# Kernel tuning notes

Hardware: AMD Instinct MI355X
Metric: run time of the kernel (lower is better)

The kernel has to match this reference:

```python
import jax, jax.numpy as jnp
import numpy as np

H = 2048          # hidden_size
M = 512           # moe_intermediate_size
E = 8             # n_routed_experts
TOP_K = 2         # num_experts_per_tok
N_SHARED = 2      # n_shared_experts -> shared intermediate = M * N_SHARED
MS = M * N_SHARED
B, S = 2, 1024


def setup_inputs() -> dict:
    key = jax.random.key(0)
    ks = jax.random.split(key, 9)
    sc = 0.02
    return {
        "hidden_states": jax.random.normal(ks[0], (B, S, H), dtype=jnp.float32),
        "gate_w": jax.random.normal(ks[1], (E, H), dtype=jnp.float32) * sc,
        "Wg": jax.random.normal(ks[2], (E, H, M), dtype=jnp.float32) * sc,   # gate_proj per expert
        "Wu": jax.random.normal(ks[3], (E, H, M), dtype=jnp.float32) * sc,   # up_proj per expert
        "Wd": jax.random.normal(ks[4], (E, M, H), dtype=jnp.float32) * sc,   # down_proj per expert
        "sWg": jax.random.normal(ks[5], (H, MS), dtype=jnp.float32) * sc,    # shared gate_proj
        "sWu": jax.random.normal(ks[6], (H, MS), dtype=jnp.float32) * sc,    # shared up_proj
        "sWd": jax.random.normal(ks[7], (MS, H), dtype=jnp.float32) * sc,    # shared down_proj
    }


def reference(hidden_states, gate_w, Wg, Wu, Wd, sWg, sWu, sWd):
    b, s, h = hidden_states.shape
    x = hidden_states.reshape(-1, h)                     # [N, H]
    n = x.shape[0]

    # --- MoEGate: top-k routing with softmax over the selected logits ---
    logits = x @ gate_w.T                                # [N, E]
    topk_vals, topk_idx = jax.lax.top_k(logits, TOP_K)   # [N, K]
    w = jax.nn.softmax(topk_vals, axis=-1)               # softmax scoring over top-k
    # per-token combine weight for every expert (zero where not routed)
    comb = jnp.zeros((n, E), x.dtype).at[jnp.arange(n)[:, None], topk_idx].add(w)

    # --- Routed experts (SwiGLU MLP per expert); combine is the sparse
    #     weight matrix `comb`, mathematically identical to torch dispatch ---
    g = jnp.einsum('nh,ehm->enm', x, Wg)                 # [E, N, M]
    u = jnp.einsum('nh,ehm->enm', x, Wu)
    eo = jnp.einsum('enm,emh->enh', jax.nn.silu(g) * u, Wd)  # [E, N, H]
    y = jnp.einsum('ne,enh->nh', comb, eo)               # weighted combine

    # --- Shared experts (dense SwiGLU MLP on all tokens) ---
    y = y + (jax.nn.silu(x @ sWg) * (x @ sWu)) @ sWd
    return y.reshape(b, s, h)
```

## Files before the change

### kernel.cpp

```cpp
#include <hip/hip_runtime.h>

#define H 2048
#define MDIM 512
#define NE 8
#define MS 1024
#define NTOK 2048
#define ACT_R_ROWS 5120

typedef unsigned short u16;
typedef __attribute__((ext_vector_type(4))) short s16x4;
typedef __attribute__((ext_vector_type(8))) short s16x8;
typedef __attribute__((ext_vector_type(4))) float f32x4;

__device__ inline u16 f2bf(float f) {
  unsigned u = __builtin_bit_cast(unsigned, f);
  u = (u + 0x7fffu + ((u >> 16) & 1u)) >> 16;
  return (u16)u;
}
__device__ inline float bf2f(u16 v) {
  return __builtin_bit_cast(float, (unsigned)v << 16);
}

__device__ inline f32x4 mfma16(s16x8 a, s16x8 b, f32x4 c) {
  return __builtin_amdgcn_mfma_f32_16x16x32_bf16(a, b, c, 0, 0, 0);
}

__device__ inline void gload16(const void* g, void* l) {
  __builtin_amdgcn_global_load_lds(
      (const __attribute__((address_space(1))) unsigned int*)g,
      (__attribute__((address_space(3))) unsigned int*)l, 16, 0, 0);
}


__device__ inline void tile_t64(const float* __restrict__ src, u16* __restrict__ dst,
                                int R, int C, int bx, int by, u16 (*tt)[66]) {
  int c0 = bx * 64, r0 = by * 64;
  int t = threadIdx.x;
  int cq = (t & 15) * 4, rr = t >> 4;
  #pragma unroll
  for (int i = 0; i < 4; i++) {
    int row = rr + i * 16;
    f32x4 v = *(const f32x4*)&src[(long)(r0 + row) * C + c0 + cq];
    tt[cq + 0][row] = f2bf(v[0]);
    tt[cq + 1][row] = f2bf(v[1]);
    tt[cq + 2][row] = f2bf(v[2]);
    tt[cq + 3][row] = f2bf(v[3]);
  }
  __syncthreads();
  int c = t >> 2, ch = t & 3;
  #pragma unroll
  for (int h = 0; h < 2; h++) {
    int chunk = ch + h * 4;
    const u16* p = &tt[c][chunk * 8];
    s16x8 o;
    #pragma unroll
    for (int w0 = 0; w0 < 8; w0++) o[w0] = (short)p[w0];
    *(s16x8*)&dst[(long)(c0 + c) * R + r0 + chunk * 8] = o;
  }
}

__global__ __launch_bounds__(256) void k_front(
    const float* __restrict__ x, const float* __restrict__ gw,
    u16* __restrict__ xbf, int* __restrict__ te, float* __restrict__ tw,
    const float* __restrict__ Wg, const float* __restrict__ Wu,
    const float* __restrict__ Wd, const float* __restrict__ sWg,
    const float* __restrict__ sWu, const float* __restrict__ sWd,
    u16* __restrict__ WgT, u16* __restrict__ WuT, u16* __restrict__ WdT,
    u16* __restrict__ sWgT, u16* __restrict__ sWuT, u16* __restrict__ sWdT) {
  __shared__ u16 tt[64][66];
  int blk = blockIdx.x;
  if (blk < NTOK / 4) {
    int n = blk * 4 + (threadIdx.x >> 6);
    int lane = threadIdx.x & 63;
    double acc[NE];
    #pragma unroll
    for (int e = 0; e < NE; e++) acc[e] = 0.0;
    const f32x4* xr = (const f32x4*)(x + (size_t)n * H);
    s16x4* xo = (s16x4*)(xbf + (size_t)n * H);
    #pragma unroll
    for (int it = 0; it < H / 256; it++) {
      int j4 = it * 64 + lane;
      f32x4 v = xr[j4];
      s16x4 o;
      o[0] = (short)f2bf(v[0]); o[1] = (short)f2bf(v[1]);
      o[2] = (short)f2bf(v[2]); o[3] = (short)f2bf(v[3]);
      xo[j4] = o;
      #pragma unroll
      for (int e = 0; e < NE; e++) {
        f32x4 g = *(const f32x4*)&gw[e * H + j4 * 4];
        acc[e] += (double)v[0] * g[0] + (double)v[1] * g[1] +
                  (double)v[2] * g[2] + (double)v[3] * g[3];
      }
    }
    #pragma unroll
    for (int off = 32; off; off >>= 1) {
      #pragma unroll
      for (int e = 0; e < NE; e++) acc[e] += __shfl_xor(acc[e], off);
    }
    if (lane == 0) {
      int b0 = 0; double v0 = acc[0];
      #pragma unroll
      for (int e = 1; e < NE; e++) { if (acc[e] > v0) { v0 = acc[e]; b0 = e; } }
      int b1 = -1; double v1 = -1e300;
      #pragma unroll
      for (int e = 0; e < NE; e++) { if (e != b0 && acc[e] > v1) { v1 = acc[e]; b1 = e; } }
      double ex = exp(v1 - v0);
      te[n * 2] = b0; te[n * 2 + 1] = b1;
      tw[n * 2] = (float)(1.0 / (1.0 + ex));
      tw[n * 2 + 1] = (float)(ex / (1.0 + ex));
    }
    return;
  }
  int b = blk - NTOK / 4;
  const float* src; u16* dst; int R, C, lb;
  if (b < 2048) {
    lb = b; R = H; C = MDIM;
    int z = lb >> 8; lb &= 255;
    src = Wg + (size_t)z * H * MDIM; dst = WgT + (size_t)z * MDIM * H;
  } else if (b < 4096) {
    lb = b - 2048; R = H; C = MDIM;
    int z = lb >> 8; lb &= 255;
    src = Wu + (size_t)z * H * MDIM; dst = WuT + (size_t)z * MDIM * H;
  } else if (b < 6144) {
    lb = b - 4096; R = MDIM; C = H;
    int z = lb >> 8; lb &= 255;
    src = Wd + (size_t)z * MDIM * H; dst = WdT + (size_t)z * H * MDIM;
  } else if (b < 6656) {
    lb = b - 6144; R = H; C = MS; src = sWg; dst = sWgT;
  } else if (b < 7168) {
    lb = b - 6656; R = H; C = MS; src = sWu; dst = sWuT;
  } else {
    lb = b - 7168; R = MS; C = H; src = sWd; dst = sWdT;
  }
  int nbx = C >> 6;
  tile_t64(src, dst, R, C, lb % nbx, lb / nbx, tt);
}

__global__ __launch_bounds__(256) void k_build(
    const int* __restrict__ te, const float* __restrict__ tw,
    int* __restrict__ counts, int* __restrict__ offs,
    int* __restrict__ perm, float* __restrict__ wgt, int* __restrict__ slotmap) {
  __shared__ int cnt[256][NE];
  __shared__ int pb[NE];
  int t = threadIdx.x;
  int ebuf[16];
  int lc[NE];
  #pragma unroll
  for (int e = 0; e < NE; e++) lc[e] = 0;
  #pragma unroll
  for (int i = 0; i < 16; i++) {
    int ei = te[t * 16 + i];
    ebuf[i] = ei;
    #pragma unroll
    for (int e = 0; e < NE; e++) lc[e] += (ei == e) ? 1 : 0;
  }
  #pragma unroll
  for (int e = 0; e < NE; e++) cnt[t][e] = lc[e];
  __syncthreads();
  if (t < NE) {
    int run = 0;
    for (int i = 0; i < 256; i++) { int v = cnt[i][t]; cnt[i][t] = run; run += v; }
    counts[t] = run;
  }
  __syncthreads();
  if (t == 0) {
    int off = 0;
    #pragma unroll
    for (int e = 0; e < NE; e++) {
      pb[e] = off; offs[e] = off;
      off += ((counts[e] + 127) >> 7) << 7;
    }
    offs[NE] = off;
  }
  for (int i = t; i < ACT_R_ROWS; i += 256) { perm[i] = 0; wgt[i] = 0.f; }
  __syncthreads();
  int run2[NE];
  #pragma unroll
  for (int e = 0; e < NE; e++) run2[e] = cnt[t][e];
  #pragma unroll
  for (int i = 0; i < 16; i++) {
    int ei = ebuf[i];
    int idx = 0;
    #pragma unroll
    for (int e = 0; e < NE; e++) {
      if (ei == e) idx = pb[e] + run2[e];
      run2[e] += (ei == e) ? 1 : 0;
    }
    perm[idx] = (t * 16 + i) >> 1;
    wgt[idx] = tw[t * 16 + i];
    slotmap[t * 16 + i] = idx;
  }
}

__global__ __launch_bounds__(256, 2) void k_gu(
    const u16* __restrict__ xbf, const u16* __restrict__ WgT, const u16* __restrict__ WuT,
    const u16* __restrict__ sWgT, const u16* __restrict__ sWuT,
    u16* __restrict__ act_s, u16* __restrict__ act_r,
    const int* __restrict__ perm, const int* __restrict__ counts,
    const int* __restrict__ offs) {
  int lin = blockIdx.x;
  int xcd = lin & 7, jj = lin >> 3;
  int g = xcd + 8 * (jj % 10);
  int bx = jj / 10;
  const u16 *Bg, *Bu;
  u16* act;
  int Nout, cnt, rowBase, by;
  bool gather;
  if (g < 16) {
    gather = false; by = g;
    cnt = NTOK; rowBase = bx * 128;
    Bg = sWgT + (size_t)by * 64 * H;
    Bu = sWuT + (size_t)by * 64 * H;
    act = act_s; Nout = MS;
  } else {
    gather = true;
    int e = (g - 16) >> 3; by = (g - 16) & 7;
    cnt = counts[e];
    if (bx * 128 >= cnt) return;
    rowBase = offs[e] + bx * 128;
    Bg = WgT + ((size_t)e * MDIM + (size_t)by * 64) * H;
    Bu = WuT + ((size_t)e * MDIM + (size_t)by * 64) * H;
    act = act_r; Nout = MDIM;
  }

  __shared__ char lds[2][32768];

  int tid = threadIdx.x;
  int wave = tid >> 6, lane = tid & 63;
  int wr = wave >> 1, wc = wave & 1;
  int la = lane & 15, ks = lane >> 4;

  int rIn = tid >> 3;
  int csrc = ((tid & 7) << 4) ^ ((rIn & 7) << 4);
  const char* srcA[4];
  const char* srcBg[2];
  const char* srcBu[2];
  #pragma unroll
  for (int j = 0; j < 4; j++) {
    int row = j * 32 + rIn;
    int tok = gather ? perm[rowBase + row] : (rowBase + row);
    srcA[j] = (const char*)xbf + (size_t)tok * H * 2 + csrc;
  }
  #pragma unroll
  for (int j = 0; j < 2; j++) {
    int row = j * 32 + rIn;
    srcBg[j] = (const char*)Bg + (size_t)row * H * 2 + csrc;
    srcBu[j] = (const char*)Bu + (size_t)row * H * 2 + csrc;
  }

  int offA[4][2], offB[2][2];
  #pragma unroll
  for (int m = 0; m < 4; m++) {
    int arow = wr * 64 + m * 16 + la;
    #pragma unroll
    for (int kk = 0; kk < 2; kk++) {
      int c = kk * 64 + ks * 16;
      offA[m][kk] = arow * 128 + (c ^ ((arow & 7) << 4));
    }
  }
  #pragma unroll
  for (int n = 0; n < 2; n++) {
    int brow = wc * 32 + n * 16 + la;
    #pragma unroll
    for (int kk = 0; kk < 2; kk++) {
      int c = kk * 64 + ks * 16;
      offB[n][kk] = brow * 128 + (c ^ ((brow & 7) << 4));
    }
  }

  f32x4 zero4 = {0.f, 0.f, 0.f, 0.f};
  f32x4 gacc[4][2], uacc[4][2];
  #pragma unroll
  for (int m = 0; m < 4; m++)
    #pragma unroll
    for (int n = 0; n < 2; n++) { gacc[m][n] = zero4; uacc[m][n] = zero4; }

  auto STAGE = [&](int p, int k0) {
    char* b = lds[p];
    #pragma unroll
    for (int j = 0; j < 4; j++)
      gload16(srcA[j] + k0, b + j * 4096 + wave * 1024);
    #pragma unroll
    for (int j = 0; j < 2; j++) {
      gload16(srcBg[j] + k0, b + 16384 + j * 4096 + wave * 1024);
      gload16(srcBu[j] + k0, b + 24576 + j * 4096 + wave * 1024);
    }
  };

  const int NT = H / 64;
  STAGE(0, 0);
  STAGE(1, 128);
  asm volatile("s_waitcnt vmcnt(8)" ::: "memory");
  __builtin_amdgcn_sched_barrier(0);
  __builtin_amdgcn_s_barrier();

  for (int t = 0; t < NT; ++t) {
    int p = t & 1;
    const char* A = lds[p];
    const char* G = lds[p] + 16384;
    const char* U = lds[p] + 24576;
    s16x8 af[2][4], gf[2][2], uf[2][2];
    #pragma unroll
    for (int kk = 0; kk < 2; kk++) {
      #pragma unroll
      for (int m = 0; m < 4; m++) af[kk][m] = *(const s16x8*)(A + offA[m][kk]);
      #pragma unroll
      for (int n = 0; n < 2; n++) {
        gf[kk][n] = *(const s16x8*)(G + offB[n][kk]);
        uf[kk][n] = *(const s16x8*)(U + offB[n][kk]);
      }
    }
    asm volatile("s_waitcnt lgkmcnt(0)" ::: "memory");
    __builtin_amdgcn_sched_barrier(0);
    __builtin_amdgcn_s_barrier();
    if (t + 2 < NT) STAGE(p, (t + 2) * 128);
    __builtin_amdgcn_sched_barrier(0);
    __builtin_amdgcn_s_setprio(1);
    #pragma unroll
    for (int kk = 0; kk < 2; kk++) {
      #pragma unroll
      for (int m = 0; m < 4; m++) {
        #pragma unroll
        for (int n = 0; n < 2; n++) {
          gacc[m][n] = mfma16(af[kk][m], gf[kk][n], gacc[m][n]);
          uacc[m][n] = mfma16(af[kk][m], uf[kk][n], uacc[m][n]);
        }
      }
    }
    __builtin_amdgcn_s_setprio(0);
    if (t + 2 < NT) { asm volatile("s_waitcnt vmcnt(8)" ::: "memory"); }
    else            { asm volatile("s_waitcnt vmcnt(0)" ::: "memory"); }
    __builtin_amdgcn_sched_barrier(0);
    __builtin_amdgcn_s_barrier();
  }

  #pragma unroll
  for (int m = 0; m < 4; m++) {
    #pragma unroll
    for (int n = 0; n < 2; n++) {
      #pragma unroll
      for (int r = 0; r < 4; r++) {
        int lr = wr * 64 + m * 16 + ks * 4 + r;
        int col = by * 64 + wc * 32 + n * 16 + la;
        float gg = gacc[m][n][r], uu = uacc[m][n][r];
        float a = gg / (1.0f + __expf(-gg)) * uu;
        if (gather && (bx * 128 + lr) >= cnt) a = 0.0f;
        act[(size_t)(rowBase + lr) * Nout + col] = f2bf(a);
      }
    }
  }
}

__global__ __launch_bounds__(256, 3) void k_down2(
    const u16* __restrict__ act_s, const u16* __restrict__ act_r,
    const u16* __restrict__ sWdT, const u16* __restrict__ WdT,
    float* __restrict__ y, u16* __restrict__ rdown,
    const float* __restrict__ wgt,
    const int* __restrict__ counts, const int* __restrict__ offs) {
  int lin = blockIdx.x;
  int xcd = lin & 7, jj = lin >> 3;
  int g = xcd + 8 * (jj % 36);
  int bx = jj / 36;
  const u16 *A, *B;
  int KD, NT, cnt, rowBase, by;
  bool routed;
  if (g < 32) {
    routed = false; by = g;
    KD = MS; NT = MS / 64;
    cnt = NTOK; rowBase = bx * 128;
    A = act_s + (size_t)rowBase * MS;
    B = sWdT + (size_t)by * 64 * MS;
  } else {
    routed = true;
    int e = (g - 32) >> 5; by = (g - 32) & 31;
    KD = MDIM; NT = MDIM / 64;
    cnt = counts[e];
    if (bx * 128 >= cnt) return;
    rowBase = offs[e] + bx * 128;
    A = act_r + (size_t)rowBase * MDIM;
    B = WdT + ((size_t)e * H + (size_t)by * 64) * MDIM;
  }

  __shared__ char lds[2][24576];

  int tid = threadIdx.x;
  int wave = tid >> 6, lane = tid & 63;
  int wr = wave >> 1, wc = wave & 1;
  int la = lane & 15, ks = lane >> 4;

  int rIn = tid >> 3;
  int csrc = ((tid & 7) << 4) ^ ((rIn & 7) << 4);
  const char* srcA[4];
  const char* srcB[2];
  #pragma unroll
  for (int j = 0; j < 4; j++) {
    int row = j * 32 + rIn;
    srcA[j] = (const char*)A + (size_t)row * KD * 2 + csrc;
  }
  #pragma unroll
  for (int j = 0; j < 2; j++) {
    int row = j * 32 + rIn;
    srcB[j] = (const char*)B + (size_t)row * KD * 2 + csrc;
  }

  int offA[4][2], offB[2][2];
  #pragma unroll
  for (int m = 0; m < 4; m++) {
    int arow = wr * 64 + m * 16 + la;
    #pragma unroll
    for (int kk = 0; kk < 2; kk++) {
      int c = kk * 64 + ks * 16;
      offA[m][kk] = arow * 128 + (c ^ ((arow & 7) << 4));
    }
  }
  #pragma unroll
  for (int n = 0; n < 2; n++) {
    int brow = wc * 32 + n * 16 + la;
    #pragma unroll
    for (int kk = 0; kk < 2; kk++) {
      int c = kk * 64 + ks * 16;
      offB[n][kk] = brow * 128 + (c ^ ((brow & 7) << 4));
    }
  }

  f32x4 zero4 = {0.f, 0.f, 0.f, 0.f};
  f32x4 acc[4][2];
  #pragma unroll
  for (int m = 0; m < 4; m++)
    #pragma unroll
    for (int n = 0; n < 2; n++) acc[m][n] = zero4;

  auto STAGE = [&](int p, int k0) {
    char* b = lds[p];
    #pragma unroll
    for (int j = 0; j < 4; j++)
      gload16(srcA[j] + k0, b + j * 4096 + wave * 1024);
    #pragma unroll
    for (int j = 0; j < 2; j++)
      gload16(srcB[j] + k0, b + 16384 + j * 4096 + wave * 1024);
  };

  STAGE(0, 0);
  STAGE(1, 128);
  asm volatile("s_waitcnt vmcnt(6)" ::: "memory");
  __builtin_amdgcn_sched_barrier(0);
  __builtin_amdgcn_s_barrier();

  for (int t = 0; t < NT; ++t) {
    int p = t & 1;
    const char* Ab = lds[p];
    const char* Bb = lds[p] + 16384;
    s16x8 af[2][4], bf[2][2];
    #pragma unroll
    for (int kk = 0; kk < 2; kk++) {
      #pragma unroll
      for (int m = 0; m < 4; m++) af[kk][m] = *(const s16x8*)(Ab + offA[m][kk]);
      #pragma unroll
      for (int n = 0; n < 2; n++) bf[kk][n] = *(const s16x8*)(Bb + offB[n][kk]);
    }
    asm volatile("s_waitcnt lgkmcnt(0)" ::: "memory");
    __builtin_amdgcn_sched_barrier(0);
    __builtin_amdgcn_s_barrier();
    if (t + 2 < NT) STAGE(p, (t + 2) * 128);
    __builtin_amdgcn_sched_barrier(0);
    __builtin_amdgcn_s_setprio(1);
    #pragma unroll
    for (int kk = 0; kk < 2; kk++) {
      #pragma unroll
      for (int m = 0; m < 4; m++)
        #pragma unroll
        for (int n = 0; n < 2; n++) acc[m][n] = mfma16(af[kk][m], bf[kk][n], acc[m][n]);
    }
    __builtin_amdgcn_s_setprio(0);
    if (t + 2 < NT) { asm volatile("s_waitcnt vmcnt(6)" ::: "memory"); }
    else            { asm volatile("s_waitcnt vmcnt(0)" ::: "memory"); }
    __builtin_amdgcn_sched_barrier(0);
    __builtin_amdgcn_s_barrier();
  }

  #pragma unroll
  for (int m = 0; m < 4; m++) {
    #pragma unroll
    for (int n = 0; n < 2; n++) {
      #pragma unroll
      for (int r = 0; r < 4; r++) {
        int lr = wr * 64 + m * 16 + ks * 4 + r;
        int col = by * 64 + wc * 32 + n * 16 + la;
        float v = acc[m][n][r];
        if (routed) {
          if (bx * 128 + lr < cnt) {
            int si = rowBase + lr;
            rdown[(size_t)si * H + col] = f2bf(wgt[si] * v);
          }
        } else {
          y[(size_t)(rowBase + lr) * H + col] = v;
        }
      }
    }
  }
}

__global__ __launch_bounds__(256) void k_combine(float* __restrict__ y,
                                                 const u16* __restrict__ rdown,
                                                 const int* __restrict__ slotmap) {
  int n = blockIdx.x;
  int s0 = slotmap[n * 2], s1 = slotmap[n * 2 + 1];
  const s16x8* r0 = (const s16x8*)(rdown + (size_t)s0 * H);
  const s16x8* r1 = (const s16x8*)(rdown + (size_t)s1 * H);
  f32x4* yp = (f32x4*)(y + (size_t)n * H);
  int t = threadIdx.x;
  s16x8 a = r0[t], b = r1[t];
  f32x4 y0 = yp[2 * t], y1 = yp[2 * t + 1];
  #pragma unroll
  for (int j = 0; j < 4; j++) {
    y0[j] += bf2f((u16)a[j]) + bf2f((u16)b[j]);
    y1[j] += bf2f((u16)a[4 + j]) + bf2f((u16)b[4 + j]);
  }
  yp[2 * t] = y0;
  yp[2 * t + 1] = y1;
}


extern "C" void kernel_launch(void* const* d_in, const int* in_sizes, int n_in,
                              void* d_out, int out_size, void* d_ws, size_t ws_size,
                              hipStream_t stream) {
  const float* x   = (const float*)d_in[0];
  const float* gw  = (const float*)d_in[1];
  const float* Wg  = (const float*)d_in[2];
  const float* Wu  = (const float*)d_in[3];
  const float* Wd  = (const float*)d_in[4];
  const float* sWg = (const float*)d_in[5];
  const float* sWu = (const float*)d_in[6];
  const float* sWd = (const float*)d_in[7];
  float* y = (float*)d_out;

  char* w = (char*)d_ws;
  auto alloc = [&](size_t bytes) {
    char* p = w;
    w += (bytes + 255) & ~(size_t)255;
    return p;
  };
  u16* xbf   = (u16*)alloc((size_t)NTOK * H * 2);
  u16* WgT   = (u16*)alloc((size_t)NE * MDIM * H * 2);
  u16* WuT   = (u16*)alloc((size_t)NE * MDIM * H * 2);
  u16* WdT   = (u16*)alloc((size_t)NE * H * MDIM * 2);
  u16* sWgT  = (u16*)alloc((size_t)MS * H * 2);
  u16* sWuT  = (u16*)alloc((size_t)MS * H * 2);
  u16* sWdT  = (u16*)alloc((size_t)H * MS * 2);
  u16* act_s = (u16*)alloc((size_t)NTOK * MS * 2);
  u16* act_r = (u16*)alloc((size_t)ACT_R_ROWS * MDIM * 2);
  u16* rdown = (u16*)alloc((size_t)ACT_R_ROWS * H * 2);
  int*   te      = (int*)alloc((size_t)NTOK * 2 * 4);
  float* tw      = (float*)alloc((size_t)NTOK * 2 * 4);
  int*   counts  = (int*)alloc(64);
  int*   offs    = (int*)alloc(64);
  int*   perm    = (int*)alloc((size_t)ACT_R_ROWS * 4);
  float* wgt     = (float*)alloc((size_t)ACT_R_ROWS * 4);
  int*   slotmap = (int*)alloc((size_t)NTOK * 2 * 4);

  k_front<<<NTOK / 4 + 7680, 256, 0, stream>>>(
      x, gw, xbf, te, tw, Wg, Wu, Wd, sWg, sWu, sWd,
      WgT, WuT, WdT, sWgT, sWuT, sWdT);

  k_build<<<1, 256, 0, stream>>>(te, tw, counts, offs, perm, wgt, slotmap);

  k_gu<<<80 * 16, 256, 0, stream>>>(
      xbf, WgT, WuT, sWgT, sWuT, act_s, act_r, perm, counts, offs);

  k_down2<<<288 * 16, 256, 0, stream>>>(
      act_s, act_r, sWdT, WdT, y, rdown, wgt, counts, offs);

  k_combine<<<NTOK, 256, 0, stream>>>(y, rdown, slotmap);
}
```

Before: 149.0 us.

## Switch GEMM kernels to 4-stage LDS ring with K=32 tiles

Both the gate/up and down GEMM kernels change from a 2-buffer, K=64-per-step pipeline to a 4-buffer ring with K=32 per step, prefetching 3 tiles ahead. This removes one barrier per iteration, since the next stage is issued into a buffer nobody is reading, and the LDS swizzle is redone for 64-byte rows. The aim is deeper latency hiding with the same LDS footprint. The cost is twice as many loop iterations with fewer MFMAs each, and the wait counts must match the deeper prefetch exactly.

Measured after the change: 159.1 us. +6.8%, slower.

```diff
diff --git a/kernel.cpp b/kernel.cpp
--- a/kernel.cpp
+++ b/kernel.cpp
@@ -223,49 +223,37 @@
     act = act_r; Nout = MDIM;
   }
 
-  __shared__ char lds[2][32768];
+  __shared__ char lds[4][16384];
 
   int tid = threadIdx.x;
   int wave = tid >> 6, lane = tid & 63;
   int wr = wave >> 1, wc = wave & 1;
   int la = lane & 15, ks = lane >> 4;
 
-  int rIn = tid >> 3;
-  int csrc = ((tid & 7) << 4) ^ ((rIn & 7) << 4);
-  const char* srcA[4];
-  const char* srcBg[2];
-  const char* srcBu[2];
-  #pragma unroll
-  for (int j = 0; j < 4; j++) {
-    int row = j * 32 + rIn;
+  const char* srcA[2];
+  #pragma unroll
+  for (int j = 0; j < 2; j++) {
+    int idx = tid + j * 256;
+    int row = idx >> 2;
+    int gc = (idx & 3) ^ ((row >> 1) & 3);
     int tok = gather ? perm[rowBase + row] : (rowBase + row);
-    srcA[j] = (const char*)xbf + (size_t)tok * H * 2 + csrc;
-  }
-  #pragma unroll
-  for (int j = 0; j < 2; j++) {
-    int row = j * 32 + rIn;
-    srcBg[j] = (const char*)Bg + (size_t)row * H * 2 + csrc;
-    srcBu[j] = (const char*)Bu + (size_t)row * H * 2 + csrc;
-  }
-
-  int offA[4][2], offB[2][2];
+    srcA[j] = (const char*)xbf + (size_t)tok * H * 2 + gc * 16;
+  }
+  int rowB = tid >> 2;
+  int gcB = (tid & 3) ^ ((rowB >> 1) & 3);
+  const char* srcBg = (const char*)Bg + (size_t)rowB * H * 2 + gcB * 16;
+  const char* srcBu = (const char*)Bu + (size_t)rowB * H * 2 + gcB * 16;
+
+  int offA[4], offB[2];
   #pragma unroll
   for (int m = 0; m < 4; m++) {
     int arow = wr * 64 + m * 16 + la;
-    #pragma unroll
-    for (int kk = 0; kk < 2; kk++) {
-      int c = kk * 64 + ks * 16;
-      offA[m][kk] = arow * 128 + (c ^ ((arow & 7) << 4));
-    }
+    offA[m] = (arow * 4 + (ks ^ ((arow >> 1) & 3))) * 16;
   }
   #pragma unroll
   for (int n = 0; n < 2; n++) {
     int brow = wc * 32 + n * 16 + la;
-    #pragma unroll
-    for (int kk = 0; kk < 2; kk++) {
-      int c = kk * 64 + ks * 16;
-      offB[n][kk] = brow * 128 + (c ^ ((brow & 7) << 4));
-    }
+    offB[n] = (brow * 4 + (ks ^ ((brow >> 1) & 3))) * 16;
   }
 
   f32x4 zero4 = {0.f, 0.f, 0.f, 0.f};
@@ -277,58 +265,44 @@
 
   auto STAGE = [&](int p, int k0) {
     char* b = lds[p];
-    #pragma unroll
-    for (int j = 0; j < 4; j++)
-      gload16(srcA[j] + k0, b + j * 4096 + wave * 1024);
-    #pragma unroll
-    for (int j = 0; j < 2; j++) {
-      gload16(srcBg[j] + k0, b + 16384 + j * 4096 + wave * 1024);
-      gload16(srcBu[j] + k0, b + 24576 + j * 4096 + wave * 1024);
-    }
+    gload16(srcA[0] + k0, b + wave * 1024);
+    gload16(srcA[1] + k0, b + 4096 + wave * 1024);
+    gload16(srcBg + k0, b + 8192 + wave * 1024);
+    gload16(srcBu + k0, b + 12288 + wave * 1024);
   };
 
-  const int NT = H / 64;
+  const int NT = H / 32;
   STAGE(0, 0);
-  STAGE(1, 128);
+  STAGE(1, 64);
+  STAGE(2, 128);
   asm volatile("s_waitcnt vmcnt(8)" ::: "memory");
   __builtin_amdgcn_sched_barrier(0);
   __builtin_amdgcn_s_barrier();
 
   for (int t = 0; t < NT; ++t) {
-    int p = t & 1;
-    const char* A = lds[p];
-    const char* G = lds[p] + 16384;
-    const char* U = lds[p] + 24576;
-    s16x8 af[2][4], gf[2][2], uf[2][2];
-    #pragma unroll
-    for (int kk = 0; kk < 2; kk++) {
-      #pragma unroll
-      for (int m = 0; m < 4; m++) af[kk][m] = *(const s16x8*)(A + offA[m][kk]);
-      #pragma unroll
-      for (int n = 0; n < 2; n++) {
-        gf[kk][n] = *(const s16x8*)(G + offB[n][kk]);
-        uf[kk][n] = *(const s16x8*)(U + offB[n][kk]);
-      }
-    }
+    const char* bufp = lds[t & 3];
+    s16x8 a[4], gf[2], uf[2];
+    #pragma unroll
+    for (int m = 0; m < 4; m++) a[m] = *(const s16x8*)(bufp + offA[m]);
+    #pragma unroll
+    for (int n = 0; n < 2; n++) {
+      gf[n] = *(const s16x8*)(bufp + 8192 + offB[n]);
+      uf[n] = *(const s16x8*)(bufp + 12288 + offB[n]);
+    }
+    if (t + 3 < NT) STAGE((t + 3) & 3, (t + 3) * 64);
     asm volatile("s_waitcnt lgkmcnt(0)" ::: "memory");
     __builtin_amdgcn_sched_barrier(0);
-    __builtin_amdgcn_s_barrier();
-    if (t + 2 < NT) STAGE(p, (t + 2) * 128);
-    __builtin_amdgcn_sched_barrier(0);
     __builtin_amdgcn_s_setprio(1);
     #pragma unroll
-    for (int kk = 0; kk < 2; kk++) {
-      #pragma unroll
-      for (int m = 0; m < 4; m++) {
-        #pragma unroll
-        for (int n = 0; n < 2; n++) {
-          gacc[m][n] = mfma16(af[kk][m], gf[kk][n], gacc[m][n]);
-          uacc[m][n] = mfma16(af[kk][m], uf[kk][n], uacc[m][n]);
-        }
+    for (int m = 0; m < 4; m++) {
+      #pragma unroll
+      for (int n = 0; n < 2; n++) {
+        gacc[m][n] = mfma16(a[m], gf[n], gacc[m][n]);
+        uacc[m][n] = mfma16(a[m], uf[n], uacc[m][n]);
       }
     }
     __builtin_amdgcn_s_setprio(0);
-    if (t + 2 < NT) { asm volatile("s_waitcnt vmcnt(8)" ::: "memory"); }
+    if (t + 3 < NT) { asm volatile("s_waitcnt vmcnt(8)" ::: "memory"); }
     else            { asm volatile("s_waitcnt vmcnt(0)" ::: "memory"); }
     __builtin_amdgcn_sched_barrier(0);
     __builtin_amdgcn_s_barrier();
@@ -366,14 +340,14 @@
   bool routed;
   if (g < 32) {
     routed = false; by = g;
-    KD = MS; NT = MS / 64;
+    KD = MS; NT = MS / 32;
     cnt = NTOK; rowBase = bx * 128;
     A = act_s + (size_t)rowBase * MS;
     B = sWdT + (size_t)by * 64 * MS;
   } else {
     routed = true;
     int e = (g - 32) >> 5; by = (g - 32) & 31;
-    KD = MDIM; NT = MDIM / 64;
+    KD = MDIM; NT = MDIM / 32;
     cnt = counts[e];
     if (bx * 128 >= cnt) return;
     rowBase = offs[e] + bx * 128;
@@ -381,46 +355,35 @@
     B = WdT + ((size_t)e * H + (size_t)by * 64) * MDIM;
   }
 
-  __shared__ char lds[2][24576];
+  __shared__ char lds[4][12288];
 
   int tid = threadIdx.x;
   int wave = tid >> 6, lane = tid & 63;
   int wr = wave >> 1, wc = wave & 1;
   int la = lane & 15, ks = lane >> 4;
 
-  int rIn = tid >> 3;
-  int csrc = ((tid & 7) << 4) ^ ((rIn & 7) << 4);
-  const char* srcA[4];
-  const char* srcB[2];
-  #pragma unroll
-  for (int j = 0; j < 4; j++) {
-    int row = j * 32 + rIn;
-    srcA[j] = (const char*)A + (size_t)row * KD * 2 + csrc;
-  }
+  const char* srcA[2];
   #pragma unroll
   for (int j = 0; j < 2; j++) {
-    int row = j * 32 + rIn;
-    srcB[j] = (const char*)B + (size_t)row * KD * 2 + csrc;
-  }
-
-  int offA[4][2], offB[2][2];
+    int idx = tid + j * 256;
+    int row = idx >> 2;
+    int gc = (idx & 3) ^ ((row >> 1) & 3);
+    srcA[j] = (const char*)A + (size_t)row * KD * 2 + gc * 16;
+  }
+  int rowB = tid >> 2;
+  int gcB = (tid & 3) ^ ((rowB >> 1) & 3);
+  const char* srcB = (const char*)B + (size_t)rowB * KD * 2 + gcB * 16;
+
+  int offA[4], offB[2];
   #pragma unroll
   for (int m = 0; m < 4; m++) {
     int arow = wr * 64 + m * 16 + la;
-    #pragma unroll
-    for (int kk = 0; kk < 2; kk++) {
-      int c = kk * 64 + ks * 16;
-      offA[m][kk] = arow * 128 + (c ^ ((arow & 7) << 4));
-    }
+    offA[m] = (arow * 4 + (ks ^ ((arow >> 1) & 3))) * 16;
   }
   #pragma unroll
   for (int n = 0; n < 2; n++) {
     int brow = wc * 32 + n * 16 + la;
-    #pragma unroll
-    for (int kk = 0; kk < 2; kk++) {
-      int c = kk * 64 + ks * 16;
-      offB[n][kk] = brow * 128 + (c ^ ((brow & 7) << 4));
-    }
+    offB[n] = (brow * 4 + (ks ^ ((brow >> 1) & 3))) * 16;
   }
 
   f32x4 zero4 = {0.f, 0.f, 0.f, 0.f};
@@ -432,47 +395,35 @@
 
   auto STAGE = [&](int p, int k0) {
     char* b = lds[p];
-    #pragma unroll
-    for (int j = 0; j < 4; j++)
-      gload16(srcA[j] + k0, b + j * 4096 + wave * 1024);
-    #pragma unroll
-    for (int j = 0; j < 2; j++)
-      gload16(srcB[j] + k0, b + 16384 + j * 4096 + wave * 1024);
+    gload16(srcA[0] + k0, b + wave * 1024);
+    gload16(srcA[1] + k0, b + 4096 + wave * 1024);
+    gload16(srcB + k0, b + 8192 + wave * 1024);
   };
 
   STAGE(0, 0);
-  STAGE(1, 128);
+  STAGE(1, 64);
+  STAGE(2, 128);
   asm volatile("s_waitcnt vmcnt(6)" ::: "memory");
   __builtin_amdgcn_sched_barrier(0);
   __builtin_amdgcn_s_barrier();
 
   for (int t = 0; t < NT; ++t) {
-    int p = t & 1;
-    const char* Ab = lds[p];
-    const char* Bb = lds[p] + 16384;
-    s16x8 af[2][4], bf[2][2];
-    #pragma unroll
-    for (int kk = 0; kk < 2; kk++) {
-      #pragma unroll
-      for (int m = 0; m < 4; m++) af[kk][m] = *(const s16x8*)(Ab + offA[m][kk]);
-      #pragma unroll
-      for (int n = 0; n < 2; n++) bf[kk][n] = *(const s16x8*)(Bb + offB[n][kk]);
-    }
+    const char* bufp = lds[t & 3];
+    s16x8 a[4], bf[2];
+    #pragma unroll
+    for (int m = 0; m < 4; m++) a[m] = *(const s16x8*)(bufp + offA[m]);
+    #pragma unroll
+    for (int n = 0; n < 2; n++) bf[n] = *(const s16x8*)(bufp + 8192 + offB[n]);
+    if (t + 3 < NT) STAGE((t + 3) & 3, (t + 3) * 64);
     asm volatile("s_waitcnt lgkmcnt(0)" ::: "memory");
     __builtin_amdgcn_sched_barrier(0);
-    __builtin_amdgcn_s_barrier();
-    if (t + 2 < NT) STAGE(p, (t + 2) * 128);
-    __builtin_amdgcn_sched_barrier(0);
     __builtin_amdgcn_s_setprio(1);
     #pragma unroll
-    for (int kk = 0; kk < 2; kk++) {
-      #pragma unroll
-      for (int m = 0; m < 4; m++)
-        #pragma unroll
-        for (int n = 0; n < 2; n++) acc[m][n] = mfma16(af[kk][m], bf[kk][n], acc[m][n]);
-    }
+    for (int m = 0; m < 4; m++)
+      #pragma unroll
+      for (int n = 0; n < 2; n++) acc[m][n] = mfma16(a[m], bf[n], acc[m][n]);
     __builtin_amdgcn_s_setprio(0);
-    if (t + 2 < NT) { asm volatile("s_waitcnt vmcnt(6)" ::: "memory"); }
+    if (t + 3 < NT) { asm volatile("s_waitcnt vmcnt(6)" ::: "memory"); }
     else            { asm volatile("s_waitcnt vmcnt(0)" ::: "memory"); }
     __builtin_amdgcn_sched_barrier(0);
     __builtin_amdgcn_s_barrier();
```

## Stagger K-loop start per block and split LDS fragment reads across two MFMA halves

Applied to the files above, without the earlier changes.

Workgroups now begin their K loop at one of two phase offsets (half of the K tiles) chosen from the block index, which spreads concurrent global reads across different address ranges and may reduce channel contention. Inside each K step, the first half's LDS fragments are waited on and consumed by MFMAs before the barrier and the next stage's global loads. The second half's reads stay in flight during that work, so LDS latency overlaps with matrix math in both the gate/up and down GEMM kernels. This raises register pressure slightly and changes the floating-point summation order.

Result: slower. 154.1 us (+3.4%).

```diff
diff --git a/kernel.cpp b/kernel.cpp
--- a/kernel.cpp
+++ b/kernel.cpp
@@ -288,8 +288,11 @@
   };
 
   const int NT = H / 64;
-  STAGE(0, 0);
-  STAGE(1, 128);
+  int phase = ((lin >> 3) & 1) * (NT / 2);
+  auto KOF = [&](int s) { int v = s + phase; if (v >= NT) v -= NT; return v * 128; };
+
+  STAGE(0, KOF(0));
+  STAGE(1, KOF(1));
   asm volatile("s_waitcnt vmcnt(8)" ::: "memory");
   __builtin_amdgcn_sched_barrier(0);
   __builtin_amdgcn_s_barrier();
@@ -301,30 +304,44 @@
     const char* U = lds[p] + 24576;
     s16x8 af[2][4], gf[2][2], uf[2][2];
     #pragma unroll
-    for (int kk = 0; kk < 2; kk++) {
-      #pragma unroll
-      for (int m = 0; m < 4; m++) af[kk][m] = *(const s16x8*)(A + offA[m][kk]);
+    for (int m = 0; m < 4; m++) af[0][m] = *(const s16x8*)(A + offA[m][0]);
+    #pragma unroll
+    for (int n = 0; n < 2; n++) {
+      gf[0][n] = *(const s16x8*)(G + offB[n][0]);
+      uf[0][n] = *(const s16x8*)(U + offB[n][0]);
+    }
+    __builtin_amdgcn_sched_barrier(0);
+    #pragma unroll
+    for (int m = 0; m < 4; m++) af[1][m] = *(const s16x8*)(A + offA[m][1]);
+    #pragma unroll
+    for (int n = 0; n < 2; n++) {
+      gf[1][n] = *(const s16x8*)(G + offB[n][1]);
+      uf[1][n] = *(const s16x8*)(U + offB[n][1]);
+    }
+    asm volatile("s_waitcnt lgkmcnt(8)" ::: "memory");
+    __builtin_amdgcn_sched_barrier(0);
+    __builtin_amdgcn_s_setprio(1);
+    #pragma unroll
+    for (int m = 0; m < 4; m++) {
       #pragma unroll
       for (int n = 0; n < 2; n++) {
-        gf[kk][n] = *(const s16x8*)(G + offB[n][kk]);
-        uf[kk][n] = *(const s16x8*)(U + offB[n][kk]);
+        gacc[m][n] = mfma16(af[0][m], gf[0][n], gacc[m][n]);
+        uacc[m][n] = mfma16(af[0][m], uf[0][n], uacc[m][n]);
       }
     }
+    __builtin_amdgcn_s_setprio(0);
     asm volatile("s_waitcnt lgkmcnt(0)" ::: "memory");
     __builtin_amdgcn_sched_barrier(0);
     __builtin_amdgcn_s_barrier();
-    if (t + 2 < NT) STAGE(p, (t + 2) * 128);
+    if (t + 2 < NT) STAGE(p, KOF(t + 2));
     __builtin_amdgcn_sched_barrier(0);
     __builtin_amdgcn_s_setprio(1);
     #pragma unroll
-    for (int kk = 0; kk < 2; kk++) {
-      #pragma unroll
-      for (int m = 0; m < 4; m++) {
-        #pragma unroll
-        for (int n = 0; n < 2; n++) {
-          gacc[m][n] = mfma16(af[kk][m], gf[kk][n], gacc[m][n]);
-          uacc[m][n] = mfma16(af[kk][m], uf[kk][n], uacc[m][n]);
-        }
+    for (int m = 0; m < 4; m++) {
+      #pragma unroll
+      for (int n = 0; n < 2; n++) {
+        gacc[m][n] = mfma16(af[1][m], gf[1][n], gacc[m][n]);
+        uacc[m][n] = mfma16(af[1][m], uf[1][n], uacc[m][n]);
       }
     }
     __builtin_amdgcn_s_setprio(0);
@@ -440,8 +457,11 @@
       gload16(srcB[j] + k0, b + 16384 + j * 4096 + wave * 1024);
   };
 
-  STAGE(0, 0);
-  STAGE(1, 128);
+  int phase = ((lin >> 3) & 1) * (NT / 2);
+  auto KOF = [&](int s) { int v = s + phase; if (v >= NT) v -= NT; return v * 128; };
+
+  STAGE(0, KOF(0));
+  STAGE(1, KOF(1));
   asm volatile("s_waitcnt vmcnt(6)" ::: "memory");
   __builtin_amdgcn_sched_barrier(0);
   __builtin_amdgcn_s_barrier();
@@ -452,25 +472,32 @@
     const char* Bb = lds[p] + 16384;
     s16x8 af[2][4], bf[2][2];
     #pragma unroll
-    for (int kk = 0; kk < 2; kk++) {
-      #pragma unroll
-      for (int m = 0; m < 4; m++) af[kk][m] = *(const s16x8*)(Ab + offA[m][kk]);
-      #pragma unroll
-      for (int n = 0; n < 2; n++) bf[kk][n] = *(const s16x8*)(Bb + offB[n][kk]);
-    }
+    for (int m = 0; m < 4; m++) af[0][m] = *(const s16x8*)(Ab + offA[m][0]);
+    #pragma unroll
+    for (int n = 0; n < 2; n++) bf[0][n] = *(const s16x8*)(Bb + offB[n][0]);
+    __builtin_amdgcn_sched_barrier(0);
+    #pragma unroll
+    for (int m = 0; m < 4; m++) af[1][m] = *(const s16x8*)(Ab + offA[m][1]);
+    #pragma unroll
+    for (int n = 0; n < 2; n++) bf[1][n] = *(const s16x8*)(Bb + offB[n][1]);
+    asm volatile("s_waitcnt lgkmcnt(6)" ::: "memory");
+    __builtin_amdgcn_sched_barrier(0);
+    __builtin_amdgcn_s_setprio(1);
+    #pragma unroll
+    for (int m = 0; m < 4; m++)
+      #pragma unroll
+      for (int n = 0; n < 2; n++) acc[m][n] = mfma16(af[0][m], bf[0][n], acc[m][n]);
+    __builtin_amdgcn_s_setprio(0);
     asm volatile("s_waitcnt lgkmcnt(0)" ::: "memory");
     __builtin_amdgcn_sched_barrier(0);
     __builtin_amdgcn_s_barrier();
-    if (t + 2 < NT) STAGE(p, (t + 2) * 128);
+    if (t + 2 < NT) STAGE(p, KOF(t + 2));
     __builtin_amdgcn_sched_barrier(0);
     __builtin_amdgcn_s_setprio(1);
     #pragma unroll
-    for (int kk = 0; kk < 2; kk++) {
-      #pragma unroll
-      for (int m = 0; m < 4; m++)
-        #pragma unroll
-        for (int n = 0; n < 2; n++) acc[m][n] = mfma16(af[kk][m], bf[kk][n], acc[m][n]);
-    }
+    for (int m = 0; m < 4; m++)
+      #pragma unroll
+      for (int n = 0; n < 2; n++) acc[m][n] = mfma16(af[1][m], bf[1][n], acc[m][n]);
     __builtin_amdgcn_s_setprio(0);
     if (t + 2 < NT) { asm volatile("s_waitcnt vmcnt(6)" ::: "memory"); }
     else            { asm volatile("s_waitcnt vmcnt(0)" ::: "memory"); }
```

## Widen down-projection tile to 128x128 and split LDS reads across two k-halves

Applied to the files above, without the earlier changes.

The down-projection kernel now computes 128x128 output tiles instead of 128x64, which halves the number of blocks and doubles the accumulators per wave (4x4 MFMA tiles). Each A tile is reused across twice as many output columns, which cuts global and LDS traffic per flop. The LDS fragment reads are split into two k-halves, with a partial lgkmcnt wait so the first MFMA batch can start while the second half is still loading. The trade-off is more registers and LDS per block (launch bound lowered to 2 blocks per CU) and fewer blocks to fill the GPU.

Result: faster. 144.1 us (-3.3%).

```diff
diff --git a/kernel.cpp b/kernel.cpp
--- a/kernel.cpp
+++ b/kernel.cpp
@@ -351,7 +351,7 @@
   }
 }
 
-__global__ __launch_bounds__(256, 3) void k_down2(
+__global__ __launch_bounds__(256, 2) void k_down2(
     const u16* __restrict__ act_s, const u16* __restrict__ act_r,
     const u16* __restrict__ sWdT, const u16* __restrict__ WdT,
     float* __restrict__ y, u16* __restrict__ rdown,
@@ -359,29 +359,29 @@
     const int* __restrict__ counts, const int* __restrict__ offs) {
   int lin = blockIdx.x;
   int xcd = lin & 7, jj = lin >> 3;
-  int g = xcd + 8 * (jj % 36);
-  int bx = jj / 36;
+  int g = xcd + 8 * (jj % 18);
+  int bx = jj / 18;
   const u16 *A, *B;
   int KD, NT, cnt, rowBase, by;
   bool routed;
-  if (g < 32) {
+  if (g < 16) {
     routed = false; by = g;
     KD = MS; NT = MS / 64;
     cnt = NTOK; rowBase = bx * 128;
     A = act_s + (size_t)rowBase * MS;
-    B = sWdT + (size_t)by * 64 * MS;
+    B = sWdT + (size_t)by * 128 * MS;
   } else {
     routed = true;
-    int e = (g - 32) >> 5; by = (g - 32) & 31;
+    int e = (g - 16) >> 4; by = (g - 16) & 15;
     KD = MDIM; NT = MDIM / 64;
     cnt = counts[e];
     if (bx * 128 >= cnt) return;
     rowBase = offs[e] + bx * 128;
     A = act_r + (size_t)rowBase * MDIM;
-    B = WdT + ((size_t)e * H + (size_t)by * 64) * MDIM;
-  }
-
-  __shared__ char lds[2][24576];
+    B = WdT + ((size_t)e * H + (size_t)by * 128) * MDIM;
+  }
+
+  __shared__ char lds[2][32768];
 
   int tid = threadIdx.x;
   int wave = tid >> 6, lane = tid & 63;
@@ -390,45 +390,33 @@
 
   int rIn = tid >> 3;
   int csrc = ((tid & 7) << 4) ^ ((rIn & 7) << 4);
-  const char* srcA[4];
-  const char* srcB[2];
+  const char *srcA[4], *srcB[4];
   #pragma unroll
   for (int j = 0; j < 4; j++) {
     int row = j * 32 + rIn;
     srcA[j] = (const char*)A + (size_t)row * KD * 2 + csrc;
-  }
-  #pragma unroll
-  for (int j = 0; j < 2; j++) {
-    int row = j * 32 + rIn;
     srcB[j] = (const char*)B + (size_t)row * KD * 2 + csrc;
   }
 
-  int offA[4][2], offB[2][2];
+  int offA[4][2], offB[4][2];
   #pragma unroll
   for (int m = 0; m < 4; m++) {
     int arow = wr * 64 + m * 16 + la;
+    int brow = wc * 64 + m * 16 + la;
     #pragma unroll
     for (int kk = 0; kk < 2; kk++) {
       int c = kk * 64 + ks * 16;
       offA[m][kk] = arow * 128 + (c ^ ((arow & 7) << 4));
-    }
-  }
-  #pragma unroll
-  for (int n = 0; n < 2; n++) {
-    int brow = wc * 32 + n * 16 + la;
-    #pragma unroll
-    for (int kk = 0; kk < 2; kk++) {
-      int c = kk * 64 + ks * 16;
-      offB[n][kk] = brow * 128 + (c ^ ((brow & 7) << 4));
+      offB[m][kk] = brow * 128 + (c ^ ((brow & 7) << 4));
     }
   }
 
   f32x4 zero4 = {0.f, 0.f, 0.f, 0.f};
-  f32x4 acc[4][2];
+  f32x4 acc[4][4];
   #pragma unroll
   for (int m = 0; m < 4; m++)
     #pragma unroll
-    for (int n = 0; n < 2; n++) acc[m][n] = zero4;
+    for (int n = 0; n < 4; n++) acc[m][n] = zero4;
 
   auto STAGE = [&](int p, int k0) {
     char* b = lds[p];
@@ -436,13 +424,13 @@
     for (int j = 0; j < 4; j++)
       gload16(srcA[j] + k0, b + j * 4096 + wave * 1024);
     #pragma unroll
-    for (int j = 0; j < 2; j++)
+    for (int j = 0; j < 4; j++)
       gload16(srcB[j] + k0, b + 16384 + j * 4096 + wave * 1024);
   };
 
   STAGE(0, 0);
   STAGE(1, 128);
-  asm volatile("s_waitcnt vmcnt(6)" ::: "memory");
+  asm volatile("s_waitcnt vmcnt(8)" ::: "memory");
   __builtin_amdgcn_sched_barrier(0);
   __builtin_amdgcn_s_barrier();
 
@@ -450,14 +438,23 @@
     int p = t & 1;
     const char* Ab = lds[p];
     const char* Bb = lds[p] + 16384;
-    s16x8 af[2][4], bf[2][2];
-    #pragma unroll
-    for (int kk = 0; kk < 2; kk++) {
-      #pragma unroll
-      for (int m = 0; m < 4; m++) af[kk][m] = *(const s16x8*)(Ab + offA[m][kk]);
-      #pragma unroll
-      for (int n = 0; n < 2; n++) bf[kk][n] = *(const s16x8*)(Bb + offB[n][kk]);
-    }
+    s16x8 a0[4], b0[4], a1[4], b1[4];
+    #pragma unroll
+    for (int m = 0; m < 4; m++) a0[m] = *(const s16x8*)(Ab + offA[m][0]);
+    #pragma unroll
+    for (int n = 0; n < 4; n++) b0[n] = *(const s16x8*)(Bb + offB[n][0]);
+    #pragma unroll
+    for (int m = 0; m < 4; m++) a1[m] = *(const s16x8*)(Ab + offA[m][1]);
+    #pragma unroll
+    for (int n = 0; n < 4; n++) b1[n] = *(const s16x8*)(Bb + offB[n][1]);
+    asm volatile("s_waitcnt lgkmcnt(8)" ::: "memory");
+    __builtin_amdgcn_sched_barrier(0);
+    __builtin_amdgcn_s_setprio(1);
+    #pragma unroll
+    for (int m = 0; m < 4; m++)
+      #pragma unroll
+      for (int n = 0; n < 4; n++) acc[m][n] = mfma16(a0[m], b0[n], acc[m][n]);
+    __builtin_amdgcn_s_setprio(0);
     asm volatile("s_waitcnt lgkmcnt(0)" ::: "memory");
     __builtin_amdgcn_sched_barrier(0);
     __builtin_amdgcn_s_barrier();
@@ -465,35 +462,36 @@
     __builtin_amdgcn_sched_barrier(0);
     __builtin_amdgcn_s_setprio(1);
     #pragma unroll
-    for (int kk = 0; kk < 2; kk++) {
-      #pragma unroll
-      for (int m = 0; m < 4; m++)
+    for (int m = 0; m < 4; m++)
+      #pragma unroll
+      for (int n = 0; n < 4; n++) acc[m][n] = mfma16(a1[m], b1[n], acc[m][n]);
+    __builtin_amdgcn_s_setprio(0);
+    if (t + 2 < NT) { asm volatile("s_waitcnt vmcnt(8)" ::: "memory"); }
+    else            { asm volatile("s_waitcnt vmcnt(0)" ::: "memory"); }
+    __builtin_amdgcn_sched_barrier(0);
+    __builtin_amdgcn_s_barrier();
+  }
+
+  #pragma unroll
+  for (int m = 0; m < 4; m++) {
+    #pragma unroll
+    for (int r = 0; r < 4; r++) {
+      int lr = wr * 64 + m * 16 + ks * 4 + r;
+      if (routed) {
+        if (bx * 128 + lr < cnt) {
+          int si = rowBase + lr;
+          float wv = wgt[si];
+          #pragma unroll
+          for (int n = 0; n < 4; n++) {
+            int col = by * 128 + wc * 64 + n * 16 + la;
+            rdown[(size_t)si * H + col] = f2bf(wv * acc[m][n][r]);
+          }
+        }
+      } else {
         #pragma unroll
-        for (int n = 0; n < 2; n++) acc[m][n] = mfma16(af[kk][m], bf[kk][n], acc[m][n]);
-    }
-    __builtin_amdgcn_s_setprio(0);
-    if (t + 2 < NT) { asm volatile("s_waitcnt vmcnt(6)" ::: "memory"); }
-    else            { asm volatile("s_waitcnt vmcnt(0)" ::: "memory"); }
-    __builtin_amdgcn_sched_barrier(0);
-    __builtin_amdgcn_s_barrier();
-  }
-
-  #pragma unroll
-  for (int m = 0; m < 4; m++) {
-    #pragma unroll
-    for (int n = 0; n < 2; n++) {
-      #pragma unroll
-      for (int r = 0; r < 4; r++) {
-        int lr = wr * 64 + m * 16 + ks * 4 + r;
-        int col = by * 64 + wc * 32 + n * 16 + la;
-        float v = acc[m][n][r];
-        if (routed) {
-          if (bx * 128 + lr < cnt) {
-            int si = rowBase + lr;
-            rdown[(size_t)si * H + col] = f2bf(wgt[si] * v);
-          }
-        } else {
-          y[(size_t)(rowBase + lr) * H + col] = v;
+        for (int n = 0; n < 4; n++) {
+          int col = by * 128 + wc * 64 + n * 16 + la;
+          y[(size_t)(rowBase + lr) * H + col] = acc[m][n][r];
         }
       }
     }
@@ -567,7 +565,7 @@
   k_gu<<<80 * 16, 256, 0, stream>>>(
       xbf, WgT, WuT, sWgT, sWuT, act_s, act_r, perm, counts, offs);
 
-  k_down2<<<288 * 16, 256, 0, stream>>>(
+  k_down2<<<8 * 18 * 16, 256, 0, stream>>>(
       act_s, act_r, sWdT, WdT, y, rdown, wgt, counts, offs);
 
   k_combine<<<NTOK, 256, 0, stream>>>(y, rdown, slotmap);
```
